# Performance work log

Hardware: AMD Instinct MI355X
Metric: run time of the kernel (lower is better)

The kernel has to match this reference:

```python
import jax, jax.numpy as jnp
import numpy as np

B, C, H, S, DC = 32768, 1024, 1024, 8, 64  # batch, num_classes, hidden_dim, num_styles, calibrator dim

def setup_inputs() -> dict:
    key = jax.random.key(0)
    ks = jax.random.split(key, 12)
    inp = {
        "logits": jax.random.normal(ks[0], (B, C), dtype=jnp.float32),
        "style_idx": jax.random.randint(ks[1], (B,), 0, S, dtype=jnp.int32),
        # learned params
        "style_emb": jax.random.normal(ks[2], (S, H), dtype=jnp.float32),
        "Wa1": jax.random.normal(ks[3], (C + H, H), dtype=jnp.float32) * (1.0 / np.sqrt(C + H)),
        "ba1": jnp.zeros((H,), dtype=jnp.float32),
        "Wa2": jax.random.normal(ks[4], (H, C), dtype=jnp.float32) * (1.0 / np.sqrt(H)),
        "ba2": jnp.zeros((C,), dtype=jnp.float32),
        # per-style confidence calibrators: Linear(C,64) -> ReLU -> Linear(64,1) -> Sigmoid
        "Wc1": jax.random.normal(ks[5], (S, C, DC), dtype=jnp.float32) * (1.0 / np.sqrt(C)),
        "bc1": jnp.zeros((S, DC), dtype=jnp.float32),
        "Wc2": jax.random.normal(ks[6], (S, DC), dtype=jnp.float32) * (1.0 / np.sqrt(DC)),
        "bc2": jnp.zeros((S,), dtype=jnp.float32),
    }
    return inp

def reference(logits, style_idx, style_emb, Wa1, ba1, Wa2, ba2, Wc1, bc1, Wc2, bc2):
    # style embedding lookup + adapter MLP (residual on logits)
    emb = style_emb[style_idx]                                  # (B, H)
    combined = jnp.concatenate([logits, emb], axis=1)           # (B, C+H)
    hidden = jax.nn.relu(combined @ Wa1 + ba1)                  # (B, H)
    adjusted_logits = logits + hidden @ Wa2 + ba2               # (B, C)
    probs = jax.nn.softmax(adjusted_logits, axis=1)             # (B, C)
    # expert-routed confidence calibration: compute all styles densely, select per sample
    h = jax.nn.relu(jnp.einsum('bc,scd->bsd', probs, Wc1) + bc1)   # (B, S, DC)
    conf_all = jax.nn.sigmoid(jnp.einsum('bsd,sd->bs', h, Wc2) + bc2)  # (B, S)
    calibrated_confidence = jnp.take_along_axis(conf_all, style_idx[:, None].astype(jnp.int32), axis=1)  # (B, 1)
    return adjusted_logits, calibrated_confidence
```

## Files before the change

### kernel.cpp

```cpp
#include <hip/hip_runtime.h>
#include <hip/hip_bf16.h>
#include <stdint.h>

typedef __hip_bfloat16 bf16;
typedef __attribute__((ext_vector_type(8))) short short8;
typedef __attribute__((ext_vector_type(4))) float f32x4;

#define NB 32768
#define NC 1024
#define NH 1024
#define NS 8
#define NDC 64
#define MAXBLK 264

__device__ __forceinline__ void gload_lds16(const void* g, void* l) {
    __builtin_amdgcn_global_load_lds((const __attribute__((address_space(1))) void*)g,
                                     (__attribute__((address_space(3))) void*)l, 16, 0, 0);
}

__device__ __forceinline__ short f2bf(float x) {
    bf16 h = __float2bfloat16(x);
    short s;
    __builtin_memcpy(&s, &h, 2);
    return s;
}

__global__ __launch_bounds__(256) void convert_kernel(
    const float* __restrict__ in, bf16* __restrict__ out)
{
    const size_t i = ((size_t)blockIdx.x * 256 + threadIdx.x) * 8;
    float4 a = *(const float4*)(in + i);
    float4 b = *(const float4*)(in + i + 4);
    short8 v;
    v[0] = f2bf(a.x); v[1] = f2bf(a.y); v[2] = f2bf(a.z); v[3] = f2bf(a.w);
    v[4] = f2bf(b.x); v[5] = f2bf(b.y); v[6] = f2bf(b.z); v[7] = f2bf(b.w);
    *(short8*)((short*)out + i) = v;
}

__global__ __launch_bounds__(256) void transpose_kernel(
    const float* __restrict__ in, bf16* __restrict__ out,
    int R, int Ccols, long long in_bs, long long out_bs)
{
    __shared__ float tile[32][33];
    const float* inb = in + (long long)blockIdx.z * in_bs;
    bf16* outb = out + (long long)blockIdx.z * out_bs;
    int c0 = blockIdx.x * 32, r0 = blockIdx.y * 32;
    int tx = threadIdx.x, ty = threadIdx.y;
#pragma unroll
    for (int i = 0; i < 32; i += 8)
        tile[ty + i][tx] = inb[(size_t)(r0 + ty + i) * Ccols + c0 + tx];
    __syncthreads();
#pragma unroll
    for (int i = 0; i < 32; i += 8)
        outb[(size_t)(c0 + ty + i) * R + r0 + tx] = __float2bfloat16(tile[tx][ty + i]);
}

__global__ __launch_bounds__(256) void style_partial_kernel(
    const float* __restrict__ style_emb, const float* __restrict__ Wa1,
    float* __restrict__ partial)
{
    const int h = (blockIdx.x & 3) * 256 + threadIdx.x;
    const int ks = blockIdx.x >> 2;
    float acc[NS];
#pragma unroll
    for (int s = 0; s < NS; ++s) acc[s] = 0.f;
#pragma unroll
    for (int kk = 0; kk < 16; ++kk) {
        const int k = ks * 16 + kk;
        const float w = Wa1[(size_t)(NC + k) * NH + h];
#pragma unroll
        for (int s = 0; s < NS; ++s)
            acc[s] += style_emb[s * NH + k] * w;
    }
#pragma unroll
    for (int s = 0; s < NS; ++s)
        partial[((size_t)ks * NS + s) * NH + h] = acc[s];
}

__global__ __launch_bounds__(256) void style_reduce_kernel(
    const float* __restrict__ partial, const float* __restrict__ ba1,
    float* __restrict__ out)
{
    const int i = blockIdx.x * 256 + threadIdx.x;
    const int h = i & (NH - 1);
    const int s = i >> 10;
    float acc = ba1[h];
#pragma unroll 8
    for (int ks = 0; ks < 64; ++ks)
        acc += partial[((size_t)ks * NS + s) * NH + h];
    out[i] = acc;
}

template<int MODE>
__global__ __launch_bounds__(256, 2) void gemm_kernel(
    const bf16* __restrict__ A, const bf16* __restrict__ BT,
    bf16* __restrict__ Cb, float* __restrict__ Cf,
    int N, int K,
    const float* __restrict__ style_contrib, const int* __restrict__ style_idx,
    const float* __restrict__ resid, const float* __restrict__ bias)
{
    __shared__ short lA[128 * 32];
    __shared__ short lB[128 * 32];

    const int t = threadIdx.x;
    const int lane = t & 63;
    const int wave = t >> 6;
    const int wr = wave >> 1;
    const int wc = wave & 1;

    const int nwg = gridDim.x * gridDim.y;
    const int flat = blockIdx.y * gridDim.x + blockIdx.x;
    const int cpx = nwg >> 3;
    const int swz = (flat & 7) * cpx + (flat >> 3);
    const int bm0 = (swz / gridDim.x) * 128;
    const int bn0 = (swz % gridDim.x) * 128;

    const int r0 = t >> 2;
    const int c8 = (t & 3) * 8;

    const int mrow = lane & 15;
    const int quad = lane >> 4;

    f32x4 acc[4][4];
#pragma unroll
    for (int i = 0; i < 4; ++i)
#pragma unroll
        for (int j = 0; j < 4; ++j) acc[i][j] = (f32x4){0.f, 0.f, 0.f, 0.f};

    const bf16* gA = A + (size_t)(bm0 + r0) * K + c8;
    const bf16* gB = BT + (size_t)(bn0 + r0) * K + c8;

    for (int k0 = 0; k0 < K; k0 += 32) {
        gload_lds16(gA + k0, lA + t * 8);
        gload_lds16(gA + (size_t)64 * K + k0, lA + 2048 + t * 8);
        gload_lds16(gB + k0, lB + t * 8);
        gload_lds16(gB + (size_t)64 * K + k0, lB + 2048 + t * 8);
        __syncthreads();

        short8 af[4], bfr[4];
#pragma unroll
        for (int i = 0; i < 4; ++i)
            af[i] = *(const short8*)(lA + (wr * 64 + i * 16 + mrow) * 32 + quad * 8);
#pragma unroll
        for (int j = 0; j < 4; ++j)
            bfr[j] = *(const short8*)(lB + (wc * 64 + j * 16 + mrow) * 32 + quad * 8);
#pragma unroll
        for (int i = 0; i < 4; ++i)
#pragma unroll
            for (int j = 0; j < 4; ++j)
                acc[i][j] = __builtin_amdgcn_mfma_f32_16x16x32_bf16(af[i], bfr[j], acc[i][j], 0, 0, 0);
        __syncthreads();
    }

#pragma unroll
    for (int i = 0; i < 4; ++i) {
#pragma unroll
        for (int r = 0; r < 4; ++r) {
            const int grow = bm0 + wr * 64 + i * 16 + quad * 4 + r;
            const float* scrow = nullptr;
            const float* resrow = nullptr;
            if (MODE == 0) scrow = style_contrib + (size_t)style_idx[grow] * N;
            if (MODE == 1) resrow = resid + (size_t)grow * N;
#pragma unroll
            for (int j = 0; j < 4; ++j) {
                const int gcol = bn0 + wc * 64 + j * 16 + mrow;
                float v = acc[i][j][r];
                if (MODE == 0) {
                    v += scrow[gcol];
                    v = fmaxf(v, 0.f);
                    Cb[(size_t)grow * N + gcol] = __float2bfloat16(v);
                } else {
                    v += resrow[gcol] + bias[gcol];
                    Cf[(size_t)grow * N + gcol] = v;
                }
            }
        }
    }
}

__global__ __launch_bounds__(256) void softmax_kernel(
    const float* __restrict__ in, bf16* __restrict__ out)
{
    const size_t row = blockIdx.x;
    const float* x = in + row * NC;
    bf16* o = out + row * NC;
    const int t = threadIdx.x;
    __shared__ float red[8];

    float v[4];
    float m = -1e30f;
#pragma unroll
    for (int i = 0; i < 4; ++i) {
        v[i] = x[t + i * 256];
        m = fmaxf(m, v[i]);
    }
#pragma unroll
    for (int off = 1; off < 64; off <<= 1) m = fmaxf(m, __shfl_xor(m, off, 64));
    const int wv = t >> 6;
    if ((t & 63) == 0) red[wv] = m;
    __syncthreads();
    const float gm = fmaxf(fmaxf(red[0], red[1]), fmaxf(red[2], red[3]));

    float s = 0.f;
#pragma unroll
    for (int i = 0; i < 4; ++i) {
        v[i] = __expf(v[i] - gm);
        s += v[i];
    }
#pragma unroll
    for (int off = 1; off < 64; off <<= 1) s += __shfl_xor(s, off, 64);
    if ((t & 63) == 0) red[4 + wv] = s;
    __syncthreads();
    const float inv = 1.0f / (red[4] + red[5] + red[6] + red[7]);
#pragma unroll
    for (int i = 0; i < 4; ++i) o[t + i * 256] = __float2bfloat16(v[i] * inv);
}


__global__ __launch_bounds__(256) void hist_kernel(
    const int* __restrict__ idx, int* __restrict__ cnt)
{
    __shared__ int h[NS];
    if (threadIdx.x < NS) h[threadIdx.x] = 0;
    __syncthreads();
    atomicAdd(&h[idx[blockIdx.x * 256 + threadIdx.x]], 1);
    __syncthreads();
    if (threadIdx.x < NS) atomicAdd(&cnt[threadIdx.x], h[threadIdx.x]);
}

__global__ void plan_kernel(const int* __restrict__ cnt, int* __restrict__ cursor,
                            int* __restrict__ blk_style, int* __restrict__ blk_seg0,
                            int* __restrict__ blk_nv)
{
    if (threadIdx.x != 0 || blockIdx.x != 0) return;
    int base = 0, nb = 0;
    for (int s = 0; s < NS; ++s) {
        cursor[s] = base;
        const int c = cnt[s];
        for (int i = 0; i < c; i += 128) {
            blk_style[nb] = s;
            blk_seg0[nb] = base + i;
            blk_nv[nb] = min(128, c - i);
            ++nb;
        }
        base += c;
    }
    for (int b = nb; b < MAXBLK; ++b) { blk_style[b] = 0; blk_seg0[b] = 0; blk_nv[b] = 0; }
}

__global__ __launch_bounds__(256) void scatter_kernel(
    const int* __restrict__ idx, int* __restrict__ cursor, int* __restrict__ order)
{
    const int b = blockIdx.x * 256 + threadIdx.x;
    const int s = idx[b];
    const int lane = threadIdx.x & 63;
    int pos = 0;
#pragma unroll 1
    for (int ss = 0; ss < NS; ++ss) {
        const unsigned long long m = __ballot(s == ss);
        if (m == 0ull) continue;
        const int leader = __ffsll(m) - 1;
        int base = 0;
        if (lane == leader) base = atomicAdd(&cursor[ss], __popcll(m));
        base = __shfl(base, leader, 64);
        if (s == ss)
            pos = base + __popcll(m & ((1ull << lane) - 1ull));
    }
    order[pos] = b;
}

__global__ __launch_bounds__(256, 2) void gemm_cal_kernel(
    const bf16* __restrict__ probs, const bf16* __restrict__ Wc1T,
    const int* __restrict__ order, const int* __restrict__ blk_style,
    const int* __restrict__ blk_seg0, const int* __restrict__ blk_nv,
    const float* __restrict__ bc1, const float* __restrict__ Wc2,
    const float* __restrict__ bc2, float* __restrict__ conf_out)
{
    const int nv = blk_nv[blockIdx.x];
    if (nv == 0) return;
    const int s = blk_style[blockIdx.x];
    const int seg0 = blk_seg0[blockIdx.x];

    __shared__ short lA[128 * 32];
    __shared__ short lB[64 * 32];
    __shared__ int rid[128];

    const int t = threadIdx.x;
    const int lane = t & 63;
    const int wave = t >> 6;

    if (t < 128) rid[t] = order[seg0 + min(t, nv - 1)];
    __syncthreads();

    const int r0 = t >> 2, c8 = (t & 3) * 8;
    const bf16* gA0 = probs + (size_t)rid[r0] * NC + c8;
    const bf16* gA1 = probs + (size_t)rid[64 + r0] * NC + c8;
    const bf16* gB  = Wc1T + ((size_t)s * NDC + r0) * NC + c8;

    const int mrow = lane & 15;
    const int quad = lane >> 4;

    f32x4 acc[2][4];
#pragma unroll
    for (int i = 0; i < 2; ++i)
#pragma unroll
        for (int j = 0; j < 4; ++j) acc[i][j] = (f32x4){0.f, 0.f, 0.f, 0.f};

    for (int k0 = 0; k0 < NC; k0 += 32) {
        gload_lds16(gA0 + k0, lA + t * 8);
        gload_lds16(gA1 + k0, lA + 2048 + t * 8);
        gload_lds16(gB + k0, lB + t * 8);
        __syncthreads();

        short8 af[2], bfr[4];
#pragma unroll
        for (int i = 0; i < 2; ++i)
            af[i] = *(const short8*)(lA + (wave * 32 + i * 16 + mrow) * 32 + quad * 8);
#pragma unroll
        for (int j = 0; j < 4; ++j)
            bfr[j] = *(const short8*)(lB + (j * 16 + mrow) * 32 + quad * 8);
#pragma unroll
        for (int i = 0; i < 2; ++i)
#pragma unroll
            for (int j = 0; j < 4; ++j)
                acc[i][j] = __builtin_amdgcn_mfma_f32_16x16x32_bf16(af[i], bfr[j], acc[i][j], 0, 0, 0);
        __syncthreads();
    }

    float bcv[4], wcv[4];
#pragma unroll
    for (int j = 0; j < 4; ++j) {
        const int d = j * 16 + mrow;
        bcv[j] = bc1[s * NDC + d];
        wcv[j] = Wc2[s * NDC + d];
    }
    const float bias2 = bc2[s];
#pragma unroll
    for (int i = 0; i < 2; ++i) {
#pragma unroll
        for (int r = 0; r < 4; ++r) {
            float p = 0.f;
#pragma unroll
            for (int j = 0; j < 4; ++j) {
                const float v = acc[i][j][r] + bcv[j];
                p += fmaxf(v, 0.f) * wcv[j];
            }
#pragma unroll
            for (int off = 1; off < 16; off <<= 1) p += __shfl_xor(p, off, 64);
            const int lrow = wave * 32 + i * 16 + quad * 4 + r;
            if (mrow == 0 && lrow < nv)
                conf_out[rid[lrow]] = 1.0f / (1.0f + __expf(-(p + bias2)));
        }
    }
}

extern "C" void kernel_launch(void* const* d_in, const int* in_sizes, int n_in,
                              void* d_out, int out_size, void* d_ws, size_t ws_size,
                              hipStream_t stream) {
    const float* logits    = (const float*)d_in[0];
    const int*   style_idx = (const int*)d_in[1];
    const float* style_emb = (const float*)d_in[2];
    const float* Wa1       = (const float*)d_in[3];
    const float* ba1       = (const float*)d_in[4];
    const float* Wa2       = (const float*)d_in[5];
    const float* ba2       = (const float*)d_in[6];
    const float* Wc1       = (const float*)d_in[7];
    const float* bc1       = (const float*)d_in[8];
    const float* Wc2       = (const float*)d_in[9];
    const float* bc2       = (const float*)d_in[10];

    char* ws = (char*)d_ws;
    bf16* logits_b = (bf16*)ws;        ws += (size_t)NB * NC * 2;
    bf16* hidden = (bf16*)ws;          ws += (size_t)NB * NH * 2;
    bf16* W1T = (bf16*)ws;             ws += (size_t)NC * NH * 2;
    bf16* W2T = (bf16*)ws;             ws += (size_t)NH * NC * 2;
    bf16* Wc1T = (bf16*)ws;            ws += (size_t)NS * NDC * NC * 2;
    float* style_contrib = (float*)ws; ws += (size_t)NS * NH * 4;
    float* style_partial = (float*)ws; ws += (size_t)64 * NS * NH * 4;
    int* sty_cnt   = (int*)ws;         ws += 64;
    int* cursor    = (int*)ws;         ws += 64;
    int* order     = (int*)ws;         ws += (size_t)NB * 4;
    int* blk_style = (int*)ws;         ws += MAXBLK * 4;
    int* blk_seg0  = (int*)ws;         ws += MAXBLK * 4;
    int* blk_nv    = (int*)ws;         ws += MAXBLK * 4;

    float* adjusted = (float*)d_out;
    float* conf_out = (float*)d_out + (size_t)NB * NC;

    hipMemsetAsync(sty_cnt, 0, 64, stream);
    hist_kernel<<<NB / 256, 256, 0, stream>>>(style_idx, sty_cnt);
    plan_kernel<<<1, 64, 0, stream>>>(sty_cnt, cursor, blk_style, blk_seg0, blk_nv);
    scatter_kernel<<<NB / 256, 256, 0, stream>>>(style_idx, cursor, order);

    convert_kernel<<<(NB * NC) / (256 * 8), 256, 0, stream>>>(logits, logits_b);

    dim3 tb(32, 8);
    transpose_kernel<<<dim3(32, 32, 1), tb, 0, stream>>>(Wa1, W1T, NC, NH, 0, 0);
    transpose_kernel<<<dim3(32, 32, 1), tb, 0, stream>>>(Wa2, W2T, NH, NC, 0, 0);
    transpose_kernel<<<dim3(2, 32, NS), tb, 0, stream>>>(Wc1, Wc1T, NC, NDC,
                                                         (long long)NC * NDC, (long long)NDC * NC);
    style_partial_kernel<<<256, 256, 0, stream>>>(style_emb, Wa1, style_partial);
    style_reduce_kernel<<<NS * NH / 256, 256, 0, stream>>>(style_partial, ba1, style_contrib);

    gemm_kernel<0><<<dim3(NH / 128, NB / 128), 256, 0, stream>>>(
        logits_b, W1T, hidden, nullptr, NH, NC, style_contrib, style_idx, nullptr, nullptr);
    gemm_kernel<1><<<dim3(NC / 128, NB / 128), 256, 0, stream>>>(
        hidden, W2T, nullptr, adjusted, NC, NH, nullptr, nullptr, logits, ba2);
    softmax_kernel<<<NB, 256, 0, stream>>>(adjusted, hidden);
    gemm_cal_kernel<<<MAXBLK, 256, 0, stream>>>(hidden, Wc1T, order, blk_style, blk_seg0,
                                                blk_nv, bc1, Wc2, bc2, conf_out);
}
```

Before: 575.9 us.

## Double-buffer LDS in GEMM kernels and shrink calibrator tiles to 64 rows

Adds LDS double buffering to the main adapter GEMM and the calibrator GEMM, prefetching the next K-slice while MFMAs run on the current one, which removes one barrier per iteration. The calibrator kernel is retiled from 128 to 64 rows per block, doubling the block count (MAXBLK raised to 520) for better occupancy across CUs. This doubles LDS use per block in the main GEMM, which may cut occupancy. The calibrator now reloads the weight tile twice as often.

New measurement: 584.2 us. No clear change (+1.4%).

```diff
diff --git a/kernel.cpp b/kernel.cpp
--- a/kernel.cpp
+++ b/kernel.cpp
@@ -11,7 +11,7 @@
 #define NH 1024
 #define NS 8
 #define NDC 64
-#define MAXBLK 264
+#define MAXBLK 520
 
 __device__ __forceinline__ void gload_lds16(const void* g, void* l) {
     __builtin_amdgcn_global_load_lds((const __attribute__((address_space(1))) void*)g,
@@ -99,8 +99,8 @@
     const float* __restrict__ style_contrib, const int* __restrict__ style_idx,
     const float* __restrict__ resid, const float* __restrict__ bias)
 {
-    __shared__ short lA[128 * 32];
-    __shared__ short lB[128 * 32];
+    __shared__ short lA[2][128 * 32];
+    __shared__ short lB[2][128 * 32];
 
     const int t = threadIdx.x;
     const int lane = t & 63;
@@ -130,26 +130,37 @@
     const bf16* gA = A + (size_t)(bm0 + r0) * K + c8;
     const bf16* gB = BT + (size_t)(bn0 + r0) * K + c8;
 
+    gload_lds16(gA, lA[0] + t * 8);
+    gload_lds16(gA + (size_t)64 * K, lA[0] + 2048 + t * 8);
+    gload_lds16(gB, lB[0] + t * 8);
+    gload_lds16(gB + (size_t)64 * K, lB[0] + 2048 + t * 8);
+    __syncthreads();
+
+    int cur = 0;
     for (int k0 = 0; k0 < K; k0 += 32) {
-        gload_lds16(gA + k0, lA + t * 8);
-        gload_lds16(gA + (size_t)64 * K + k0, lA + 2048 + t * 8);
-        gload_lds16(gB + k0, lB + t * 8);
-        gload_lds16(gB + (size_t)64 * K + k0, lB + 2048 + t * 8);
-        __syncthreads();
+        const int nxt = cur ^ 1;
+        if (k0 + 32 < K) {
+            gload_lds16(gA + k0 + 32, lA[nxt] + t * 8);
+            gload_lds16(gA + (size_t)64 * K + k0 + 32, lA[nxt] + 2048 + t * 8);
+            gload_lds16(gB + k0 + 32, lB[nxt] + t * 8);
+            gload_lds16(gB + (size_t)64 * K + k0 + 32, lB[nxt] + 2048 + t * 8);
+        }
 
         short8 af[4], bfr[4];
 #pragma unroll
         for (int i = 0; i < 4; ++i)
-            af[i] = *(const short8*)(lA + (wr * 64 + i * 16 + mrow) * 32 + quad * 8);
+            af[i] = *(const short8*)(lA[cur] + (wr * 64 + i * 16 + mrow) * 32 + quad * 8);
 #pragma unroll
         for (int j = 0; j < 4; ++j)
-            bfr[j] = *(const short8*)(lB + (wc * 64 + j * 16 + mrow) * 32 + quad * 8);
+            bfr[j] = *(const short8*)(lB[cur] + (wc * 64 + j * 16 + mrow) * 32 + quad * 8);
 #pragma unroll
         for (int i = 0; i < 4; ++i)
 #pragma unroll
             for (int j = 0; j < 4; ++j)
                 acc[i][j] = __builtin_amdgcn_mfma_f32_16x16x32_bf16(af[i], bfr[j], acc[i][j], 0, 0, 0);
+
         __syncthreads();
+        cur = nxt;
     }
 
 #pragma unroll
@@ -237,10 +248,10 @@
     for (int s = 0; s < NS; ++s) {
         cursor[s] = base;
         const int c = cnt[s];
-        for (int i = 0; i < c; i += 128) {
+        for (int i = 0; i < c; i += 64) {
             blk_style[nb] = s;
             blk_seg0[nb] = base + i;
-            blk_nv[nb] = min(128, c - i);
+            blk_nv[nb] = min(64, c - i);
             ++nb;
         }
         base += c;
@@ -281,50 +292,51 @@
     const int s = blk_style[blockIdx.x];
     const int seg0 = blk_seg0[blockIdx.x];
 
-    __shared__ short lA[128 * 32];
-    __shared__ short lB[64 * 32];
-    __shared__ int rid[128];
+    __shared__ short lA[2][64 * 32];
+    __shared__ short lB[2][64 * 32];
+    __shared__ int rid[64];
 
     const int t = threadIdx.x;
     const int lane = t & 63;
     const int wave = t >> 6;
 
-    if (t < 128) rid[t] = order[seg0 + min(t, nv - 1)];
+    if (t < 64) rid[t] = order[seg0 + min(t, nv - 1)];
     __syncthreads();
 
     const int r0 = t >> 2, c8 = (t & 3) * 8;
-    const bf16* gA0 = probs + (size_t)rid[r0] * NC + c8;
-    const bf16* gA1 = probs + (size_t)rid[64 + r0] * NC + c8;
-    const bf16* gB  = Wc1T + ((size_t)s * NDC + r0) * NC + c8;
+    const bf16* gA = probs + (size_t)rid[r0] * NC + c8;
+    const bf16* gB = Wc1T + ((size_t)s * NDC + r0) * NC + c8;
 
     const int mrow = lane & 15;
     const int quad = lane >> 4;
 
-    f32x4 acc[2][4];
-#pragma unroll
-    for (int i = 0; i < 2; ++i)
-#pragma unroll
-        for (int j = 0; j < 4; ++j) acc[i][j] = (f32x4){0.f, 0.f, 0.f, 0.f};
-
+    f32x4 acc[4];
+#pragma unroll
+    for (int j = 0; j < 4; ++j) acc[j] = (f32x4){0.f, 0.f, 0.f, 0.f};
+
+    gload_lds16(gA, lA[0] + t * 8);
+    gload_lds16(gB, lB[0] + t * 8);
+    __syncthreads();
+
+    int cur = 0;
     for (int k0 = 0; k0 < NC; k0 += 32) {
-        gload_lds16(gA0 + k0, lA + t * 8);
-        gload_lds16(gA1 + k0, lA + 2048 + t * 8);
-        gload_lds16(gB + k0, lB + t * 8);
+        const int nxt = cur ^ 1;
+        if (k0 + 32 < NC) {
+            gload_lds16(gA + k0 + 32, lA[nxt] + t * 8);
+            gload_lds16(gB + k0 + 32, lB[nxt] + t * 8);
+        }
+
+        const short8 af = *(const short8*)(lA[cur] + (wave * 16 + mrow) * 32 + quad * 8);
+        short8 bfr[4];
+#pragma unroll
+        for (int j = 0; j < 4; ++j)
+            bfr[j] = *(const short8*)(lB[cur] + (j * 16 + mrow) * 32 + quad * 8);
+#pragma unroll
+        for (int j = 0; j < 4; ++j)
+            acc[j] = __builtin_amdgcn_mfma_f32_16x16x32_bf16(af, bfr[j], acc[j], 0, 0, 0);
+
         __syncthreads();
-
-        short8 af[2], bfr[4];
-#pragma unroll
-        for (int i = 0; i < 2; ++i)
-            af[i] = *(const short8*)(lA + (wave * 32 + i * 16 + mrow) * 32 + quad * 8);
-#pragma unroll
-        for (int j = 0; j < 4; ++j)
-            bfr[j] = *(const short8*)(lB + (j * 16 + mrow) * 32 + quad * 8);
-#pragma unroll
-        for (int i = 0; i < 2; ++i)
-#pragma unroll
-            for (int j = 0; j < 4; ++j)
-                acc[i][j] = __builtin_amdgcn_mfma_f32_16x16x32_bf16(af[i], bfr[j], acc[i][j], 0, 0, 0);
-        __syncthreads();
+        cur = nxt;
     }
 
     float bcv[4], wcv[4];
@@ -336,21 +348,18 @@
     }
     const float bias2 = bc2[s];
 #pragma unroll
-    for (int i = 0; i < 2; ++i) {
-#pragma unroll
-        for (int r = 0; r < 4; ++r) {
-            float p = 0.f;
-#pragma unroll
-            for (int j = 0; j < 4; ++j) {
-                const float v = acc[i][j][r] + bcv[j];
-                p += fmaxf(v, 0.f) * wcv[j];
-            }
-#pragma unroll
-            for (int off = 1; off < 16; off <<= 1) p += __shfl_xor(p, off, 64);
-            const int lrow = wave * 32 + i * 16 + quad * 4 + r;
-            if (mrow == 0 && lrow < nv)
-                conf_out[rid[lrow]] = 1.0f / (1.0f + __expf(-(p + bias2)));
+    for (int r = 0; r < 4; ++r) {
+        float p = 0.f;
+#pragma unroll
+        for (int j = 0; j < 4; ++j) {
+            const float v = acc[j][r] + bcv[j];
+            p += fmaxf(v, 0.f) * wcv[j];
         }
+#pragma unroll
+        for (int off = 1; off < 16; off <<= 1) p += __shfl_xor(p, off, 64);
+        const int lrow = wave * 16 + quad * 4 + r;
+        if (mrow == 0 && lrow < nv)
+            conf_out[rid[lrow]] = 1.0f / (1.0f + __expf(-(p + bias2)));
     }
 }
 
```
